# Optimization experiments

Hardware: AMD Instinct MI355X
Metric: run time of the kernel (lower is better)

## Reference

```python
import jax, jax.numpy as jnp
import numpy as np

N_ITER = 4  # n_iter
NEG = -1e9  # masked-score fill (softmax-safe stand-in for -inf)


def _mfvi(x, mask, ternary, global_):
    """MFVI message passing between head (H) and node (Z) variables with global nodes.

    x:       [B, L, D] unary scores for Z nodes
    mask:    [B, L]    padding mask (nonzero = valid token)
    ternary: [D, D, H] ternary factor scores f(Z_i=a, Z_j=b, H-channel c)
    global_: [G, D, H] global-node factor scores
    Defaults: norm=softmax, regularize=1, stepsize=1, damping=0, async_update,
    no tensor decomposition, mode='all-attn', block_msg=False, output_prob=False.
    """
    B, L, D = x.shape
    m1 = (mask != 0)                                             # [B, L]
    pair_valid = m1[:, None, :, None] & m1[:, None, None, :]     # [B, 1, L, L]
    unary = x                                                    # pos_embed='none'
    Qz = jax.nn.softmax(unary, axis=-1)                          # [B, L, D]
    F_Z = unary
    neg = jnp.asarray(NEG, x.dtype)
    for _ in range(N_ITER):
        # --- H update: scores for head variable H_{i,c} over candidate heads j ---
        # F_Hs[n,h,i,j] = sum_{a,b} Qz[n,i,a] * ternary[a,b,h] * Qz[n,j,b]
        F_Hs = jnp.einsum('nia,abh,njb->nhij', Qz, ternary, Qz)  # [B, H, L, L]
        F_Hs = jnp.where(pair_valid, F_Hs, neg)
        # global-node columns: F_Hg[n,h,i,g] = sum_a Qz[n,i,a] * global_[g,a,h]
        F_Hg = jnp.einsum('nia,gah->nhig', Qz, global_)          # [B, H, L, G]
        F_H = jnp.concatenate([F_Hs, F_Hg], axis=-1)             # [B, H, L, L+G]
        Q_H = jax.nn.softmax(F_H, axis=-1)                       # regularize_H = 1
        Qhs, Qhg = Q_H[..., :L], Q_H[..., L:]
        # --- Z update (async: uses fresh Q_H) ---
        # message to Z_i from its chosen head j
        msg_i = jnp.einsum('nhij,njb,abh->nia', Qhs, Qz, ternary)
        # message to Z_j from dependents i (block_msg=False keeps it)
        msg_j = jnp.einsum('nhij,nia,abh->njb', Qhs, Qz, ternary)
        # message to Z_i from global nodes
        msg_g = jnp.einsum('nhig,gah->nia', Qhg, global_)
        F_Z = unary + msg_i + msg_j + msg_g                      # [B, L, D]
        Qz = jax.nn.softmax(F_Z, axis=-1)                        # regularize_Z = 1
    # output_prob=False -> unnormalized scores, zeroed at padding
    return jnp.where(m1[..., None], F_Z, jnp.zeros_like(F_Z))


def setup_inputs() -> dict:
    key = jax.random.key(0)
    k1, k2, k3 = jax.random.split(key, 3)
    B, L, D, H, G = 4, 1024, 128, 8, 64
    x = jax.random.normal(k1, (B, L, D), dtype=jnp.float32)
    mask = jnp.ones((B, L), dtype=jnp.int32)
    ternary = jax.random.normal(k2, (D, D, H), dtype=jnp.float32)          # init std=1
    global_ = jax.random.normal(k3, (G, D, H), dtype=jnp.float32) / np.sqrt(D)
    return {"x": x, "mask": mask, "ternary": ternary, "global_": global_}


def reference(x, mask, ternary, global_):
    return _mfvi(x, mask, ternary, global_)
```

## Files before the change

kernel.cpp:

```cpp
#include <hip/hip_runtime.h>
#include <math.h>

#define Bn 4
#define Ln 1024
#define Dn 128
#define Hn 8
#define Gn 64
#define NITERS 4

typedef _Float16 f16;
typedef _Float16 half8 __attribute__((ext_vector_type(8)));
typedef _Float16 half4v __attribute__((ext_vector_type(4)));
typedef float floatx4 __attribute__((ext_vector_type(4)));

#define WPAD 136
#define UBPAD 72
#define PPAD 72

#define MFMA(a, b, c) __builtin_amdgcn_mfma_f32_16x16x32_f16((a), (b), (c), 0, 0, 0)

__global__ void repack_kernel(const float* __restrict__ ter, const float* __restrict__ glb,
                              f16* __restrict__ TpA, f16* __restrict__ TpB,
                              f16* __restrict__ GpA, f16* __restrict__ Gpt) {
    int idx = blockIdx.x * 256 + threadIdx.x;
    if (idx < Dn * Dn * Hn) {
        int h = idx % Hn; int b = (idx / Hn) % Dn; int a = idx / (Hn * Dn);
        f16 v = (f16)ter[idx];
        TpA[((size_t)h * Dn + a) * Dn + b] = v;
        TpB[((size_t)h * Dn + b) * Dn + a] = v;
    }
    if (idx < Gn * Dn * Hn) {
        int h = idx % Hn; int a = (idx / Hn) % Dn; int g = idx / (Hn * Dn);
        f16 v = (f16)glb[idx];
        GpA[((size_t)h * Gn + g) * Dn + a] = v;
        Gpt[((size_t)h * Dn + a) * Gn + g] = v;
    }
}

__global__ void softmax_rows_kernel(const float* __restrict__ in, f16* __restrict__ out) {
    int row = blockIdx.x;
    int t = threadIdx.x;
    __shared__ float red[2];
    float v = in[(size_t)row * Dn + t];
    float m = v;
    #pragma unroll
    for (int off = 1; off < 64; off <<= 1) m = fmaxf(m, __shfl_xor(m, off, 64));
    if ((t & 63) == 0) red[t >> 6] = m;
    __syncthreads();
    m = fmaxf(red[0], red[1]);
    float e = __expf(v - m);
    float s = e;
    #pragma unroll
    for (int off = 1; off < 64; off <<= 1) s += __shfl_xor(s, off, 64);
    __syncthreads();
    if ((t & 63) == 0) red[t >> 6] = s;
    __syncthreads();
    s = red[0] + red[1];
    out[(size_t)row * Dn + t] = (f16)(e / s);
}

__launch_bounds__(256, 4)
__global__ void uv_kernel(const f16* __restrict__ Qz, const f16* __restrict__ TpA,
                          const f16* __restrict__ TpB,
                          f16* __restrict__ U, f16* __restrict__ Ut, f16* __restrict__ Vt) {
    int bx = blockIdx.x;
    int h  = blockIdx.y;
    int n  = blockIdx.z;
    int t  = threadIdx.x;
    int w = t >> 6, l = t & 63, m = l & 15, q = l >> 4;

    __shared__ __align__(16) f16 Ts[128 * WPAD];

    int jrow = bx * 64 + w * 16 + m;
    const f16* qbase = Qz + ((size_t)n * Ln + jrow) * Dn;
    half8 aq[4];
    #pragma unroll
    for (int ks = 0; ks < 4; ks++)
        aq[ks] = *(const half8*)(qbase + ks * 32 + q * 8);

    size_t hoff = (size_t)(n * Hn + h);
    int jr0 = bx * 64 + w * 16 + 4 * q;

    {
        const f16* src = TpA + (size_t)h * Dn * Dn;
        for (int ii = 0; ii < 8; ii++) {
            int idx = t + 256 * ii; int r = idx >> 4, c = idx & 15;
            *(float4*)&Ts[r * WPAD + c * 8] = *(const float4*)(src + (size_t)r * Dn + c * 8);
        }
        __syncthreads();
        #pragma unroll
        for (int ct = 0; ct < 8; ct++) {
            floatx4 acc = {0.f, 0.f, 0.f, 0.f};
            #pragma unroll
            for (int ks = 0; ks < 4; ks++) {
                half8 b = *(const half8*)&Ts[(ct * 16 + m) * WPAD + ks * 32 + q * 8];
                acc = MFMA(aq[ks], b, acc);
            }
            f16* ub = U + (hoff * Ln + jr0) * Dn + ct * 16 + m;
            #pragma unroll
            for (int reg = 0; reg < 4; reg++) ub[(size_t)reg * Dn] = (f16)acc[reg];
            half4v pk = { (f16)acc[0], (f16)acc[1], (f16)acc[2], (f16)acc[3] };
            *(half4v*)(Ut + (hoff * Dn + ct * 16 + m) * Ln + jr0) = pk;
        }
        __syncthreads();
    }
    {
        const f16* src = TpB + (size_t)h * Dn * Dn;
        for (int ii = 0; ii < 8; ii++) {
            int idx = t + 256 * ii; int r = idx >> 4, c = idx & 15;
            *(float4*)&Ts[r * WPAD + c * 8] = *(const float4*)(src + (size_t)r * Dn + c * 8);
        }
        __syncthreads();
        #pragma unroll
        for (int ct = 0; ct < 8; ct++) {
            floatx4 acc = {0.f, 0.f, 0.f, 0.f};
            #pragma unroll
            for (int ks = 0; ks < 4; ks++) {
                half8 b = *(const half8*)&Ts[(ct * 16 + m) * WPAD + ks * 32 + q * 8];
                acc = MFMA(aq[ks], b, acc);
            }
            half4v pk = { (f16)acc[0], (f16)acc[1], (f16)acc[2], (f16)acc[3] };
            *(half4v*)(Vt + (hoff * Dn + ct * 16 + m) * Ln + jr0) = pk;
        }
    }
}

__launch_bounds__(256, 3)
__global__ void msgi_kernel(const f16* __restrict__ Qz, const f16* __restrict__ U,
                            const f16* __restrict__ Ut, const f16* __restrict__ GpA,
                            const f16* __restrict__ Gpt, const int* __restrict__ mask,
                            f16* __restrict__ Macc, float* __restrict__ rowLinv) {
    int it = blockIdx.x, h = blockIdx.y, n = blockIdx.z;
    int t = threadIdx.x;
    int w = t >> 6, l = t & 63, m = l & 15, q = l >> 4;
    int rh = w >> 1, ch = w & 1;
    int ih = w >> 1, ah = w & 1;

    __shared__ __align__(16) f16 Us[64 * WPAD];
    __shared__ __align__(16) f16 Ub[128 * UBPAD];
    __shared__ __align__(16) f16 Ps[64 * PPAD];
    __shared__ int jms[64];
    __shared__ float lpart[2][64];
    __shared__ float linvS[64];

    half8 bq[2][4];
    #pragma unroll
    for (int ib = 0; ib < 2; ib++) {
        const f16* qr = Qz + ((size_t)n * Ln + it * 64 + ch * 32 + ib * 16 + m) * Dn;
        #pragma unroll
        for (int ks = 0; ks < 4; ks++)
            bq[ib][ks] = *(const half8*)(qr + ks * 32 + q * 8);
    }
    int im[2];
    #pragma unroll
    for (int ib = 0; ib < 2; ib++)
        im[ib] = mask[n * Ln + it * 64 + ch * 32 + ib * 16 + m];

    float lacc[2] = {0.f, 0.f};
    floatx4 Oacc[2][4];
    #pragma unroll
    for (int ib = 0; ib < 2; ib++)
        #pragma unroll
        for (int at = 0; at < 4; at++) Oacc[ib][at] = (floatx4){0.f, 0.f, 0.f, 0.f};

    size_t hoff = (size_t)(n * Hn + h);

    for (int jt = 0; jt < 17; jt++) {
        int isg = (jt == 16);
        const f16* us; const f16* ub; int ustr;
        if (!isg) {
            us = U + (hoff * Ln + (size_t)jt * 64) * Dn;
            ub = Ut + hoff * Dn * Ln + jt * 64;
            ustr = Ln;
        } else {
            us = GpA + (size_t)h * Gn * Dn;
            ub = Gpt + (size_t)h * Dn * Gn;
            ustr = Gn;
        }
        __syncthreads();
        #pragma unroll
        for (int ii = 0; ii < 4; ii++) {
            int idx = t + 256 * ii;
            float4 v = *(const float4*)(us + (size_t)(idx >> 4) * Dn + (idx & 15) * 8);
            *(float4*)&Us[(idx >> 4) * WPAD + (idx & 15) * 8] = v;
            float4 v2 = *(const float4*)(ub + (size_t)(idx >> 3) * ustr + (idx & 7) * 8);
            *(float4*)&Ub[(idx >> 3) * UBPAD + (idx & 7) * 8] = v2;
        }
        if (t < 64) jms[t] = isg ? 1 : mask[n * Ln + jt * 64 + t];
        __syncthreads();

        #pragma unroll
        for (int jb = 0; jb < 2; jb++) {
            half8 au[4];
            #pragma unroll
            for (int ks = 0; ks < 4; ks++)
                au[ks] = *(const half8*)&Us[(rh * 32 + jb * 16 + m) * WPAD + ks * 32 + q * 8];
            int jmr[4];
            #pragma unroll
            for (int reg = 0; reg < 4; reg++)
                jmr[reg] = jms[rh * 32 + jb * 16 + 4 * q + reg];
            #pragma unroll
            for (int ib = 0; ib < 2; ib++) {
                floatx4 s = {0.f, 0.f, 0.f, 0.f};
                #pragma unroll
                for (int ks = 0; ks < 4; ks++) s = MFMA(au[ks], bq[ib][ks], s);
                half4v pk;
                #pragma unroll
                for (int reg = 0; reg < 4; reg++) {
                    float p = (isg || (im[ib] && jmr[reg])) ? __expf(fminf(s[reg], 11.f)) : 0.f;
                    lacc[ib] += p;
                    pk[reg] = (f16)p;
                }
                *(half4v*)&Ps[(ch * 32 + ib * 16 + m) * PPAD + rh * 32 + jb * 16 + 4 * q] = pk;
            }
        }
        __syncthreads();

        #pragma unroll
        for (int kst = 0; kst < 2; kst++) {
            half8 aP[2];
            #pragma unroll
            for (int ib = 0; ib < 2; ib++)
                aP[ib] = *(const half8*)&Ps[(ih * 32 + ib * 16 + m) * PPAD + kst * 32 + q * 8];
            #pragma unroll
            for (int at = 0; at < 4; at++) {
                half8 bU = *(const half8*)&Ub[(ah * 64 + at * 16 + m) * UBPAD + kst * 32 + q * 8];
                #pragma unroll
                for (int ib = 0; ib < 2; ib++)
                    Oacc[ib][at] = MFMA(aP[ib], bU, Oacc[ib][at]);
            }
        }
    }

    #pragma unroll
    for (int ib = 0; ib < 2; ib++) {
        float v = lacc[ib];
        v += __shfl_xor(v, 16, 64);
        v += __shfl_xor(v, 32, 64);
        lacc[ib] = v;
    }
    if (q == 0) {
        lpart[rh][ch * 32 + m] = lacc[0];
        lpart[rh][ch * 32 + 16 + m] = lacc[1];
    }
    __syncthreads();
    size_t rbase = hoff * Ln + (size_t)it * 64;
    if (t < 64) {
        float inv = 1.0f / (lpart[0][t] + lpart[1][t]);
        linvS[t] = inv;
        int mk = mask[n * Ln + it * 64 + t];
        rowLinv[rbase + t] = mk ? inv : 0.f;
    }
    __syncthreads();
    f16* Mo = Macc + rbase * Dn;
    #pragma unroll
    for (int ib = 0; ib < 2; ib++)
        #pragma unroll
        for (int reg = 0; reg < 4; reg++) {
            int row = ih * 32 + ib * 16 + 4 * q + reg;
            float inv = linvS[row];
            #pragma unroll
            for (int at = 0; at < 4; at++)
                Mo[(size_t)row * Dn + ah * 64 + at * 16 + m] = (f16)(Oacc[ib][at][reg] * inv);
        }
}

__launch_bounds__(256, 3)
__global__ void msgj_kernel(const f16* __restrict__ Qz, const f16* __restrict__ U,
                            const f16* __restrict__ Vt, const int* __restrict__ mask,
                            const float* __restrict__ rowLinv, f16* __restrict__ Macc) {
    int jt = blockIdx.x, h = blockIdx.y, n = blockIdx.z;
    int t = threadIdx.x;
    int w = t >> 6, l = t & 63, m = l & 15, q = l >> 4;
    int ihs = w >> 1, jhs = w & 1;
    int jh2 = w >> 1, bh = w & 1;

    __shared__ __align__(16) f16 Qs[64 * WPAD];
    __shared__ __align__(16) f16 Vb[128 * UBPAD];
    __shared__ __align__(16) f16 Psj[64 * PPAD];
    __shared__ float lvS[64];

    size_t hoff = (size_t)(n * Hn + h);

    half8 bu[2][4];
    #pragma unroll
    for (int jb = 0; jb < 2; jb++) {
        const f16* ur = U + (hoff * Ln + (size_t)jt * 64 + jhs * 32 + jb * 16 + m) * Dn;
        #pragma unroll
        for (int ks = 0; ks < 4; ks++)
            bu[jb][ks] = *(const half8*)(ur + ks * 32 + q * 8);
    }
    int jm[2];
    #pragma unroll
    for (int jb = 0; jb < 2; jb++)
        jm[jb] = mask[n * Ln + jt * 64 + jhs * 32 + jb * 16 + m];

    floatx4 Oacc[2][4];
    #pragma unroll
    for (int jb = 0; jb < 2; jb++)
        #pragma unroll
        for (int bt = 0; bt < 4; bt++) Oacc[jb][bt] = (floatx4){0.f, 0.f, 0.f, 0.f};

    for (int it2 = 0; it2 < 16; it2++) {
        const f16* qs = Qz + ((size_t)n * Ln + it2 * 64) * Dn;
        const f16* vs = Vt + hoff * Dn * Ln + it2 * 64;
        __syncthreads();
        #pragma unroll
        for (int ii = 0; ii < 4; ii++) {
            int idx = t + 256 * ii;
            float4 v = *(const float4*)(qs + (size_t)(idx >> 4) * Dn + (idx & 15) * 8);
            *(float4*)&Qs[(idx >> 4) * WPAD + (idx & 15) * 8] = v;
            float4 v2 = *(const float4*)(vs + (size_t)(idx >> 3) * Ln + (idx & 7) * 8);
            *(float4*)&Vb[(idx >> 3) * UBPAD + (idx & 7) * 8] = v2;
        }
        if (t < 64) lvS[t] = rowLinv[hoff * Ln + it2 * 64 + t];
        __syncthreads();

        #pragma unroll
        for (int ib = 0; ib < 2; ib++) {
            half8 aq2[4];
            #pragma unroll
            for (int ks = 0; ks < 4; ks++)
                aq2[ks] = *(const half8*)&Qs[(ihs * 32 + ib * 16 + m) * WPAD + ks * 32 + q * 8];
            float lv[4];
            #pragma unroll
            for (int reg = 0; reg < 4; reg++)
                lv[reg] = lvS[ihs * 32 + ib * 16 + 4 * q + reg];
            #pragma unroll
            for (int jb = 0; jb < 2; jb++) {
                floatx4 s = {0.f, 0.f, 0.f, 0.f};
                #pragma unroll
                for (int ks = 0; ks < 4; ks++) s = MFMA(aq2[ks], bu[jb][ks], s);
                half4v pk;
                #pragma unroll
                for (int reg = 0; reg < 4; reg++) {
                    float p = jm[jb] ? __expf(fminf(s[reg], 11.f)) * lv[reg] : 0.f;
                    pk[reg] = (f16)p;
                }
                *(half4v*)&Psj[(jhs * 32 + jb * 16 + m) * PPAD + ihs * 32 + ib * 16 + 4 * q] = pk;
            }
        }
        __syncthreads();

        #pragma unroll
        for (int kst = 0; kst < 2; kst++) {
            half8 aP[2];
            #pragma unroll
            for (int jb = 0; jb < 2; jb++)
                aP[jb] = *(const half8*)&Psj[(jh2 * 32 + jb * 16 + m) * PPAD + kst * 32 + q * 8];
            #pragma unroll
            for (int bt = 0; bt < 4; bt++) {
                half8 bV = *(const half8*)&Vb[(bh * 64 + bt * 16 + m) * UBPAD + kst * 32 + q * 8];
                #pragma unroll
                for (int jb = 0; jb < 2; jb++)
                    Oacc[jb][bt] = MFMA(aP[jb], bV, Oacc[jb][bt]);
            }
        }
    }

    f16* Mo = Macc + (hoff * Ln + (size_t)jt * 64) * Dn;
    #pragma unroll
    for (int jb = 0; jb < 2; jb++)
        #pragma unroll
        for (int reg = 0; reg < 4; reg++) {
            int row = jh2 * 32 + jb * 16 + 4 * q + reg;
            #pragma unroll
            for (int bt = 0; bt < 4; bt++) {
                f16* p = &Mo[(size_t)row * Dn + bh * 64 + bt * 16 + m];
                *p = (f16)((float)*p + Oacc[jb][bt][reg]);
            }
        }
}

__global__ void combine_kernel(const float* __restrict__ x, const f16* __restrict__ Macc,
                               const int* __restrict__ mask, float* __restrict__ out,
                               f16* __restrict__ Qzh, int do_softmax, int do_mask) {
    int row = blockIdx.x;
    int t = threadIdx.x;
    __shared__ float red[2];
    int n = row >> 10;
    float acc = x[(size_t)row * Dn + t];
    const f16* mp = Macc + (size_t)n * Hn * Ln * Dn + (size_t)(row & 1023) * Dn + t;
    #pragma unroll
    for (int h = 0; h < Hn; h++) acc += (float)mp[(size_t)h * Ln * Dn];
    float o = acc;
    if (do_mask && mask[row] == 0) o = 0.f;
    out[(size_t)row * Dn + t] = o;
    if (do_softmax) {
        float m = acc;
        #pragma unroll
        for (int off = 1; off < 64; off <<= 1) m = fmaxf(m, __shfl_xor(m, off, 64));
        if ((t & 63) == 0) red[t >> 6] = m;
        __syncthreads();
        m = fmaxf(red[0], red[1]);
        float e = __expf(acc - m);
        float s = e;
        #pragma unroll
        for (int off = 1; off < 64; off <<= 1) s += __shfl_xor(s, off, 64);
        __syncthreads();
        if ((t & 63) == 0) red[t >> 6] = s;
        __syncthreads();
        s = red[0] + red[1];
        Qzh[(size_t)row * Dn + t] = (f16)(e / s);
    }
}

extern "C" void kernel_launch(void* const* d_in, const int* in_sizes, int n_in,
                              void* d_out, int out_size, void* d_ws, size_t ws_size,
                              hipStream_t stream) {
    const float* x       = (const float*)d_in[0];
    const int*   mask    = (const int*)d_in[1];
    const float* ternary = (const float*)d_in[2];
    const float* global_ = (const float*)d_in[3];
    float* out = (float*)d_out;
    (void)ws_size; (void)n_in; (void)in_sizes; (void)out_size;

    char* ws = (char*)d_ws;
    size_t o = 0;
    f16* Qzh = (f16*)(ws + o); o += (size_t)Bn * Ln * Dn * 2;
    f16* U   = (f16*)(ws + o); o += (size_t)Bn * Hn * Ln * Dn * 2;
    f16* Ut  = (f16*)(ws + o); o += (size_t)Bn * Hn * Ln * Dn * 2;
    f16* Vt  = (f16*)(ws + o); o += (size_t)Bn * Hn * Ln * Dn * 2;
    f16* TpA = (f16*)(ws + o); o += (size_t)Hn * Dn * Dn * 2;
    f16* TpB = (f16*)(ws + o); o += (size_t)Hn * Dn * Dn * 2;
    f16* GpA = (f16*)(ws + o); o += (size_t)Hn * Gn * Dn * 2;
    f16* Gpt = (f16*)(ws + o); o += (size_t)Hn * Dn * Gn * 2;
    float* rowLinv = (float*)(ws + o); o += (size_t)Bn * Hn * Ln * 4;
    f16* Macc = (f16*)(ws + o); o += (size_t)Bn * Hn * Ln * Dn * 2;

    repack_kernel<<<(Dn * Dn * Hn + 255) / 256, 256, 0, stream>>>(ternary, global_, TpA, TpB, GpA, Gpt);
    softmax_rows_kernel<<<Bn * Ln, 128, 0, stream>>>(x, Qzh);

    for (int it = 0; it < NITERS; it++) {
        uv_kernel<<<dim3(Ln / 64, Hn, Bn), 256, 0, stream>>>(Qzh, TpA, TpB, U, Ut, Vt);
        msgi_kernel<<<dim3(Ln / 64, Hn, Bn), 256, 0, stream>>>(Qzh, U, Ut, GpA, Gpt, mask, Macc, rowLinv);
        msgj_kernel<<<dim3(Ln / 64, Hn, Bn), 256, 0, stream>>>(Qzh, U, Vt, mask, rowLinv, Macc);
        combine_kernel<<<Bn * Ln, 128, 0, stream>>>(x, Macc, mask, out, Qzh,
                                                    (it < NITERS - 1) ? 1 : 0,
                                                    (it == NITERS - 1) ? 1 : 0);
    }
}
```

Baseline: 434.4 us.

## Double-buffer msg kernels with async global-to-LDS loads and XOR swizzle

Both message kernels now prefetch the next U/Ut (or Qz/Vt) tile straight into a second LDS buffer with global_load_lds while the current tile is being computed. Because these direct writes cannot use padded rows, the LDS layout switches from padding to an XOR swizzle to avoid bank conflicts. The goal is to hide global load latency and drop the register round-trip on each tile copy. The cost is roughly doubled LDS use, so launch bounds drop from 3 to 2 blocks per CU, which lowers occupancy. Correctness also relies on the barrier waiting for the async LDS writes to finish.

```diff
diff --git a/kernel.cpp b/kernel.cpp
--- a/kernel.cpp
+++ b/kernel.cpp
@@ -14,10 +14,32 @@
 typedef float floatx4 __attribute__((ext_vector_type(4)));
 
 #define WPAD 136
-#define UBPAD 72
 #define PPAD 72
 
 #define MFMA(a, b, c) __builtin_amdgcn_mfma_f32_16x16x32_f16((a), (b), (c), 0, 0, 0)
+
+__device__ __forceinline__ void gl_lds16(const f16* g, f16* l) {
+    __builtin_amdgcn_global_load_lds(
+        (const __attribute__((address_space(1))) void*)(g),
+        (__attribute__((address_space(3))) void*)(l),
+        16, 0, 0);
+}
+
+__device__ __forceinline__ void issue_tiles(const f16* us, const f16* ub, int sb,
+                                            f16* UsB, f16* UbB, int w, int l) {
+    #pragma unroll
+    for (int k = 0; k < 4; k++) {
+        int c = w * 4 + k;
+        {
+            int r = c * 4 + (l >> 4); int g = (l & 15) ^ (r & 7);
+            gl_lds16(us + (size_t)r * Dn + g * 8, UsB + c * 512);
+        }
+        {
+            int r = c * 8 + (l >> 3); int g = (l & 7) ^ (r & 7);
+            gl_lds16(ub + (size_t)r * sb + g * 8, UbB + c * 512);
+        }
+    }
+}
 
 __global__ void repack_kernel(const float* __restrict__ ter, const float* __restrict__ glb,
                               f16* __restrict__ TpA, f16* __restrict__ TpB,
@@ -125,7 +147,7 @@
     }
 }
 
-__launch_bounds__(256, 3)
+__launch_bounds__(256, 2)
 __global__ void msgi_kernel(const f16* __restrict__ Qz, const f16* __restrict__ U,
                             const f16* __restrict__ Ut, const f16* __restrict__ GpA,
                             const f16* __restrict__ Gpt, const int* __restrict__ mask,
@@ -136,10 +158,10 @@
     int rh = w >> 1, ch = w & 1;
     int ih = w >> 1, ah = w & 1;
 
-    __shared__ __align__(16) f16 Us[64 * WPAD];
-    __shared__ __align__(16) f16 Ub[128 * UBPAD];
+    __shared__ __align__(16) f16 Us[2][64 * 128];
+    __shared__ __align__(16) f16 Ub[2][128 * 64];
     __shared__ __align__(16) f16 Ps[64 * PPAD];
-    __shared__ int jms[64];
+    __shared__ int jms[2][64];
     __shared__ float lpart[2][64];
     __shared__ float linvS[64];
 
@@ -165,40 +187,38 @@
 
     size_t hoff = (size_t)(n * Hn + h);
 
+    issue_tiles(U + hoff * Ln * Dn, Ut + hoff * Dn * Ln, Ln, Us[0], Ub[0], w, l);
+    if (t < 64) jms[0][t] = mask[n * Ln + t];
+    __syncthreads();
+
     for (int jt = 0; jt < 17; jt++) {
+        int cur = jt & 1, nxt = cur ^ 1;
+        if (jt + 1 < 17) {
+            const f16 *us, *ub; int sb;
+            if (jt + 1 < 16) {
+                us = U + (hoff * Ln + (size_t)(jt + 1) * 64) * Dn;
+                ub = Ut + hoff * Dn * Ln + (jt + 1) * 64;
+                sb = Ln;
+            } else {
+                us = GpA + (size_t)h * Gn * Dn;
+                ub = Gpt + (size_t)h * Dn * Gn;
+                sb = Gn;
+            }
+            issue_tiles(us, ub, sb, Us[nxt], Ub[nxt], w, l);
+            if (t < 64) jms[nxt][t] = (jt + 1 < 16) ? mask[n * Ln + (jt + 1) * 64 + t] : 1;
+        }
         int isg = (jt == 16);
-        const f16* us; const f16* ub; int ustr;
-        if (!isg) {
-            us = U + (hoff * Ln + (size_t)jt * 64) * Dn;
-            ub = Ut + hoff * Dn * Ln + jt * 64;
-            ustr = Ln;
-        } else {
-            us = GpA + (size_t)h * Gn * Dn;
-            ub = Gpt + (size_t)h * Dn * Gn;
-            ustr = Gn;
-        }
-        __syncthreads();
-        #pragma unroll
-        for (int ii = 0; ii < 4; ii++) {
-            int idx = t + 256 * ii;
-            float4 v = *(const float4*)(us + (size_t)(idx >> 4) * Dn + (idx & 15) * 8);
-            *(float4*)&Us[(idx >> 4) * WPAD + (idx & 15) * 8] = v;
-            float4 v2 = *(const float4*)(ub + (size_t)(idx >> 3) * ustr + (idx & 7) * 8);
-            *(float4*)&Ub[(idx >> 3) * UBPAD + (idx & 7) * 8] = v2;
-        }
-        if (t < 64) jms[t] = isg ? 1 : mask[n * Ln + jt * 64 + t];
-        __syncthreads();
-
         #pragma unroll
         for (int jb = 0; jb < 2; jb++) {
+            int r0 = rh * 32 + jb * 16 + m;
             half8 au[4];
             #pragma unroll
             for (int ks = 0; ks < 4; ks++)
-                au[ks] = *(const half8*)&Us[(rh * 32 + jb * 16 + m) * WPAD + ks * 32 + q * 8];
+                au[ks] = *(const half8*)&Us[cur][((size_t)r0 << 7) + ((((ks << 2) + q)) ^ (r0 & 7)) * 8];
             int jmr[4];
             #pragma unroll
             for (int reg = 0; reg < 4; reg++)
-                jmr[reg] = jms[rh * 32 + jb * 16 + 4 * q + reg];
+                jmr[reg] = jms[cur][rh * 32 + jb * 16 + 4 * q + reg];
             #pragma unroll
             for (int ib = 0; ib < 2; ib++) {
                 floatx4 s = {0.f, 0.f, 0.f, 0.f};
@@ -224,12 +244,14 @@
                 aP[ib] = *(const half8*)&Ps[(ih * 32 + ib * 16 + m) * PPAD + kst * 32 + q * 8];
             #pragma unroll
             for (int at = 0; at < 4; at++) {
-                half8 bU = *(const half8*)&Ub[(ah * 64 + at * 16 + m) * UBPAD + kst * 32 + q * 8];
+                int r0 = ah * 64 + at * 16 + m;
+                half8 bU = *(const half8*)&Ub[cur][((size_t)r0 << 6) + ((((kst << 2) + q)) ^ (r0 & 7)) * 8];
                 #pragma unroll
                 for (int ib = 0; ib < 2; ib++)
                     Oacc[ib][at] = MFMA(aP[ib], bU, Oacc[ib][at]);
             }
         }
+        __syncthreads();
     }
 
     #pragma unroll
@@ -265,7 +287,7 @@
         }
 }
 
-__launch_bounds__(256, 3)
+__launch_bounds__(256, 2)
 __global__ void msgj_kernel(const f16* __restrict__ Qz, const f16* __restrict__ U,
                             const f16* __restrict__ Vt, const int* __restrict__ mask,
                             const float* __restrict__ rowLinv, f16* __restrict__ Macc) {
@@ -275,10 +297,10 @@
     int ihs = w >> 1, jhs = w & 1;
     int jh2 = w >> 1, bh = w & 1;
 
-    __shared__ __align__(16) f16 Qs[64 * WPAD];
-    __shared__ __align__(16) f16 Vb[128 * UBPAD];
+    __shared__ __align__(16) f16 Qs[2][64 * 128];
+    __shared__ __align__(16) f16 Vb[2][128 * 64];
     __shared__ __align__(16) f16 Psj[64 * PPAD];
-    __shared__ float lvS[64];
+    __shared__ float lvS[2][64];
 
     size_t hoff = (size_t)(n * Hn + h);
 
@@ -301,31 +323,28 @@
         #pragma unroll
         for (int bt = 0; bt < 4; bt++) Oacc[jb][bt] = (floatx4){0.f, 0.f, 0.f, 0.f};
 
+    issue_tiles(Qz + (size_t)n * Ln * Dn, Vt + hoff * Dn * Ln, Ln, Qs[0], Vb[0], w, l);
+    if (t < 64) lvS[0][t] = rowLinv[hoff * Ln + t];
+    __syncthreads();
+
     for (int it2 = 0; it2 < 16; it2++) {
-        const f16* qs = Qz + ((size_t)n * Ln + it2 * 64) * Dn;
-        const f16* vs = Vt + hoff * Dn * Ln + it2 * 64;
-        __syncthreads();
-        #pragma unroll
-        for (int ii = 0; ii < 4; ii++) {
-            int idx = t + 256 * ii;
-            float4 v = *(const float4*)(qs + (size_t)(idx >> 4) * Dn + (idx & 15) * 8);
-            *(float4*)&Qs[(idx >> 4) * WPAD + (idx & 15) * 8] = v;
-            float4 v2 = *(const float4*)(vs + (size_t)(idx >> 3) * Ln + (idx & 7) * 8);
-            *(float4*)&Vb[(idx >> 3) * UBPAD + (idx & 7) * 8] = v2;
-        }
-        if (t < 64) lvS[t] = rowLinv[hoff * Ln + it2 * 64 + t];
-        __syncthreads();
-
+        int cur = it2 & 1, nxt = cur ^ 1;
+        if (it2 + 1 < 16) {
+            issue_tiles(Qz + ((size_t)n * Ln + (size_t)(it2 + 1) * 64) * Dn,
+                        Vt + hoff * Dn * Ln + (it2 + 1) * 64, Ln, Qs[nxt], Vb[nxt], w, l);
+            if (t < 64) lvS[nxt][t] = rowLinv[hoff * Ln + (it2 + 1) * 64 + t];
+        }
         #pragma unroll
         for (int ib = 0; ib < 2; ib++) {
+            int r0 = ihs * 32 + ib * 16 + m;
             half8 aq2[4];
             #pragma unroll
             for (int ks = 0; ks < 4; ks++)
-                aq2[ks] = *(const half8*)&Qs[(ihs * 32 + ib * 16 + m) * WPAD + ks * 32 + q * 8];
+                aq2[ks] = *(const half8*)&Qs[cur][((size_t)r0 << 7) + ((((ks << 2) + q)) ^ (r0 & 7)) * 8];
             float lv[4];
             #pragma unroll
             for (int reg = 0; reg < 4; reg++)
-                lv[reg] = lvS[ihs * 32 + ib * 16 + 4 * q + reg];
+                lv[reg] = lvS[cur][ihs * 32 + ib * 16 + 4 * q + reg];
             #pragma unroll
             for (int jb = 0; jb < 2; jb++) {
                 floatx4 s = {0.f, 0.f, 0.f, 0.f};
@@ -350,12 +369,14 @@
                 aP[jb] = *(const half8*)&Psj[(jh2 * 32 + jb * 16 + m) * PPAD + kst * 32 + q * 8];
             #pragma unroll
             for (int bt = 0; bt < 4; bt++) {
-                half8 bV = *(const half8*)&Vb[(bh * 64 + bt * 16 + m) * UBPAD + kst * 32 + q * 8];
+                int r0 = bh * 64 + bt * 16 + m;
+                half8 bV = *(const half8*)&Vb[cur][((size_t)r0 << 6) + ((((kst << 2) + q)) ^ (r0 & 7)) * 8];
                 #pragma unroll
                 for (int jb = 0; jb < 2; jb++)
                     Oacc[jb][bt] = MFMA(aP[jb], bV, Oacc[jb][bt]);
             }
         }
+        __syncthreads();
     }
 
     f16* Mo = Macc + (hoff * Ln + (size_t)jt * 64) * Dn;
```

Result: faster. 395.1 us (-9.0%).
